# Performance work log

Hardware: AMD Instinct MI355X
Metric: run time of the kernel (lower is better)

## Reference

```python
import jax, jax.numpy as jnp
import numpy as np

B, D, N, K = 4, 1024, 2048, 1024
INIT_STD = 0.05  # keras 'random_normal' initializer default stddev


def setup_inputs() -> dict:
    key = jax.random.key(0)
    kx, kq, kk, kv, ko = jax.random.split(key, 5)
    inputs = jax.random.normal(kx, (B, D, N), dtype=jnp.float32)
    W_Q = jax.random.normal(kq, (K, D), dtype=jnp.float32) * INIT_STD
    W_K = jax.random.normal(kk, (K, D), dtype=jnp.float32) * INIT_STD
    W_V = jax.random.normal(kv, (K, D), dtype=jnp.float32) * INIT_STD
    W_O = jax.random.normal(ko, (K, D), dtype=jnp.float32) * INIT_STD
    return {"inputs": inputs, "W_Q": W_Q, "W_K": W_K, "W_V": W_V, "W_O": W_O}


def reference(inputs, W_Q, W_K, W_V, W_O):
    # inputs: (b, d, n) -- feature-major layout, sequence on the last axis.
    b, d, n = inputs.shape
    # Q/K projections fused into a single bilinear form: (W_Q x_i) . (W_K x_j)
    # logits[b, i, j] = x[:, i]^T W_Q^T W_K x[:, j]
    q = jnp.einsum('kd,bdi->bki', W_Q, inputs)          # (b, k, n)
    kk = jnp.einsum('kd,bdj->bkj', W_K, inputs)         # (b, k, n)
    logits = jnp.einsum('bki,bkj->bij', q, kk)          # (b, n, n)
    # Causal mask D: -inf strictly above the diagonal (query i attends j <= i).
    causal = jnp.tril(jnp.ones((n, n), dtype=bool))
    logits = jnp.where(causal, logits, -jnp.inf)
    A = jax.nn.softmax(logits, axis=-1)                 # (b, n_q, n_k)
    # context[:, :, i] = sum_t x[:, :, t] * A[i, t]
    ctx = jnp.einsum('bet,bit->bei', inputs, A)         # (b, d, n)
    # Residual + fused V/O projection: x + W_O^T W_V x A
    out = inputs + jnp.einsum('kd,ke,bei->bdi', W_O, W_V, ctx)
    return out
```

## Files before the change

kernel.cpp:

```cpp
#include <hip/hip_runtime.h>
#include <hip/hip_bf16.h>
#include <math.h>

#define BB 4
#define DD 1024
#define NN 2048
#define KK 1024
#define NT128 16
#define NTRI 136
#define TRI_ELEMS 16384

typedef __attribute__((ext_vector_type(4))) float f32x4;
typedef __attribute__((ext_vector_type(8))) short bfrag;

typedef __attribute__((address_space(1))) const unsigned int gu32;
typedef __attribute__((address_space(3))) unsigned int lu32;

__device__ __forceinline__ void async16(const void* g, void* l) {
  __builtin_amdgcn_global_load_lds((gu32*)g, (lu32*)l, 16, 0, 0);
}

__device__ __forceinline__ ushort f2b(float f) {
  union { float f; unsigned u; } c; c.f = f;
  unsigned u = c.u + 0x7fffu + ((c.u >> 16) & 1u);
  return (ushort)(u >> 16);
}
__device__ __forceinline__ float b2f(ushort h) {
  union { unsigned u; float f; } c; c.u = ((unsigned)h) << 16;
  return c.f;
}

__global__ __launch_bounds__(256) void prep(
    const float* __restrict__ x,
    const float* __restrict__ WQ, const float* __restrict__ WK,
    const float* __restrict__ WV, const float* __restrict__ WO,
    ushort* __restrict__ xhi, ushort* __restrict__ xTh, ushort* __restrict__ xTl,
    ushort* __restrict__ qh, ushort* __restrict__ ql,
    ushort* __restrict__ kh, ushort* __restrict__ kl_,
    ushort* __restrict__ vh, ushort* __restrict__ oh) {
  const int z = blockIdx.z;
  const int tx = threadIdx.x, ty = threadIdx.y;
  __shared__ float tile[32][33];
  if (z < 4) {
    const int b = z;
    const int n0 = blockIdx.x * 32, d0 = blockIdx.y * 32;
    const float* xb = x + (long)b * DD * NN;
    ushort* xhb = xhi + (long)b * DD * NN;
#pragma unroll
    for (int r = 0; r < 4; ++r) {
      const int dl = ty + r * 8;
      const float v = xb[(long)(d0 + dl) * NN + n0 + tx];
      tile[dl][tx] = v;
      xhb[(long)(d0 + dl) * NN + n0 + tx] = f2b(v);
    }
    __syncthreads();
#pragma unroll
    for (int r = 0; r < 4; ++r) {
      const int nl = ty + r * 8;
      const float v = tile[tx][nl];
      const ushort h = f2b(v);
      const long o = (long)b * NN * DD + (long)(n0 + nl) * DD + d0 + tx;
      xTh[o] = h;
      xTl[o] = f2b(v - b2f(h));
    }
  } else {
    const int w = (z - 4) * 2 + (blockIdx.x >> 5);
    const float* W = (w == 0) ? WQ : (w == 1) ? WK : (w == 2) ? WV : WO;
    ushort* Th = (w == 0) ? qh : (w == 1) ? kh : (w == 2) ? vh : oh;
    ushort* Tl = (w == 0) ? ql : (w == 1) ? kl_ : nullptr;
    const int k0 = (blockIdx.x & 31) * 32, d0 = blockIdx.y * 32;
#pragma unroll
    for (int r = 0; r < 4; ++r) {
      const int kl = ty + r * 8;
      tile[kl][tx] = W[(long)(k0 + kl) * DD + d0 + tx];
    }
    __syncthreads();
#pragma unroll
    for (int r = 0; r < 4; ++r) {
      const int dl = ty + r * 8;
      const float v = tile[tx][dl];
      const ushort h = f2b(v);
      const long o = (long)(d0 + dl) * KK + k0 + tx;
      Th[o] = h;
      if (Tl) Tl[o] = f2b(v - b2f(h));
    }
  }
}

__global__ __launch_bounds__(256) void gemm_w(
    const ushort* __restrict__ qh, const ushort* __restrict__ ql,
    const ushort* __restrict__ kh, const ushort* __restrict__ kl_,
    const ushort* __restrict__ vh, const ushort* __restrict__ oh,
    ushort* __restrict__ mqk_h, ushort* __restrict__ mqk_l,
    ushort* __restrict__ mov_h) {
  extern __shared__ ushort smem[];
  ushort* sAh = smem;
  ushort* sAl = smem + 2048;
  ushort* sBh = smem + 4096;
  ushort* sBl = smem + 6144;

  const int id = blockIdx.x;
  const int half = id >> 8;
  const int t = id & 255;
  const int m0 = (t >> 4) * 64, n0 = (t & 15) * 64;
  const ushort* A_h = half ? oh : qh;
  const ushort* B_h = half ? vh : kh;

  const int tid = threadIdx.x;
  const int lane = tid & 63, wave = tid >> 6;
  const int wm = (wave & 1) * 32, wn = (wave >> 1) * 32;
  const int r16 = lane & 15, quad = lane >> 4;
  const int kc = ((lane & 3) ^ ((lane >> 3) & 3)) * 8;
  const int srow = lane >> 2;

  f32x4 acc[2][2];
#pragma unroll
  for (int i = 0; i < 2; ++i)
#pragma unroll
    for (int j = 0; j < 2; ++j) acc[i][j] = (f32x4){0.f, 0.f, 0.f, 0.f};

  for (int k0 = 0; k0 < KK; k0 += 32) {
    __syncthreads();
    {
      const int row = wave * 16 + srow;
      const long aoff = (long)(m0 + row) * KK + k0 + kc;
      const long boff = (long)(n0 + row) * KK + k0 + kc;
      async16(A_h + aoff, sAh + wave * 512);
      async16(B_h + boff, sBh + wave * 512);
      if (half == 0) {
        async16(ql + aoff, sAl + wave * 512);
        async16(kl_ + boff, sBl + wave * 512);
      }
    }
    __syncthreads();

    const int sw = (r16 >> 1) & 3;
    bfrag ah[2], bh[2], al[2], bl[2];
#pragma unroll
    for (int t2 = 0; t2 < 2; ++t2) {
      ah[t2] = *(const bfrag*)&sAh[(wm + t2 * 16 + r16) * 32 + (quad ^ sw) * 8];
      bh[t2] = *(const bfrag*)&sBh[(wn + t2 * 16 + r16) * 32 + (quad ^ sw) * 8];
      if (half == 0) {
        al[t2] = *(const bfrag*)&sAl[(wm + t2 * 16 + r16) * 32 + (quad ^ sw) * 8];
        bl[t2] = *(const bfrag*)&sBl[(wn + t2 * 16 + r16) * 32 + (quad ^ sw) * 8];
      }
    }
#pragma unroll
    for (int mt = 0; mt < 2; ++mt)
#pragma unroll
      for (int nt = 0; nt < 2; ++nt) {
        acc[mt][nt] = __builtin_amdgcn_mfma_f32_16x16x32_bf16(ah[mt], bh[nt], acc[mt][nt], 0, 0, 0);
        if (half == 0) {
          acc[mt][nt] = __builtin_amdgcn_mfma_f32_16x16x32_bf16(ah[mt], bl[nt], acc[mt][nt], 0, 0, 0);
          acc[mt][nt] = __builtin_amdgcn_mfma_f32_16x16x32_bf16(al[mt], bh[nt], acc[mt][nt], 0, 0, 0);
        }
      }
  }

#pragma unroll
  for (int mt = 0; mt < 2; ++mt)
#pragma unroll
    for (int nt = 0; nt < 2; ++nt)
#pragma unroll
      for (int reg = 0; reg < 4; ++reg) {
        const int ml = wm + mt * 16 + quad * 4 + reg;
        const int nl = wn + nt * 16 + r16;
        const float v = acc[mt][nt][reg];
        const long o = (long)(m0 + ml) * DD + n0 + nl;
        if (half == 0) {
          const ushort h = f2b(v);
          mqk_h[o] = h;
          mqk_l[o] = f2b(v - b2f(h));
        } else {
          mov_h[o] = f2b(v);
        }
      }
}

template <int SPLIT, int TRIA, int STORE, int SWIZ>
__global__ __launch_bounds__(256) void gemm_mfma(
    const ushort* __restrict__ Ah, const ushort* __restrict__ Al,
    const ushort* __restrict__ Bh, const ushort* __restrict__ Bl,
    void* __restrict__ C0, void* __restrict__ C1, const float* __restrict__ Res,
    int K, int lda, int ldb, int ldc,
    long bA, long bB, long bC, long bR) {
  extern __shared__ ushort smem[];

  int b, m0, n0, tiC = 0;
  if (SWIZ == 2) {
    const int g = (blockIdx.x & 7) * 68 + (blockIdx.x >> 3);
    b = g / NTRI;
    int t = g - b * NTRI;
    int ti = 0;
    while ((ti + 1) * (ti + 2) / 2 <= t) ++ti;
    const int tj = t - ti * (ti + 1) / 2;
    m0 = ti * 128; n0 = tj * 128; tiC = t;
  } else if (SWIZ == 1) {
    const int g = (blockIdx.x & 7) * 64 + (blockIdx.x >> 3);
    const int P = g >> 3;
    b = P >> 4;
    m0 = (P & 15) * 128;
    n0 = (g & 7) * 128;
  } else if (SWIZ == 3) {
    const int xcd = blockIdx.x & 7;
    const int idx = blockIdx.x >> 3;
    const int q = idx >> 3;
    b = q >> 1;
    const int mt_ = (q & 1) ? (15 - xcd) : xcd;
    m0 = mt_ * 128;
    n0 = (idx & 7) * 128;
  } else {
    const int g = (blockIdx.x & 7) * 64 + (blockIdx.x >> 3);
    const int P = g >> 3;
    b = P >> 4;
    n0 = (P & 15) * 128;
    m0 = (g & 7) * 128;
  }
  const int kmax = TRIA ? (m0 + 128) : K;
  int triA0 = 0;
  if (TRIA) { const int ti = m0 >> 7; triA0 = ti * (ti + 1) / 2; }

  const ushort* A_h = Ah + (long)b * bA;
  const ushort* B_h = Bh + (long)b * bB;
  const ushort* A_l = SPLIT ? Al + (long)b * bA : nullptr;
  const ushort* B_l = SPLIT ? Bl + (long)b * bB : nullptr;

  const int tid = threadIdx.x;
  const int lane = tid & 63, wave = tid >> 6;
  const int wm = (wave & 1) * 64, wn = (wave >> 1) * 64;
  const int r16 = lane & 15, quad = lane >> 4;
  const int rk = r16 & 7;

  const int lrow = lane >> 3;
  const int lc = (lane & 7) ^ lrow;
  const int lckS = (lc & 3) * 8;
  const bool lo_src = lc >= 4;
  const int kcP = lc * 8;

  f32x4 acc[4][4];
#pragma unroll
  for (int i = 0; i < 4; ++i)
#pragma unroll
    for (int j = 0; j < 4; ++j) acc[i][j] = (f32x4){0.f, 0.f, 0.f, 0.f};

  auto STAGE = [&](int db, int t) {
    ushort* dst = smem + db * 16384;
    if (SPLIT) {
      const int k0 = t << 5;
#pragma unroll
      for (int s = 0; s < 4; ++s) {
        const int seg = wave * 4 + s;
        const int row = seg * 8 + lrow;
        const ushort* baseA = lo_src ? A_l : A_h;
        const ushort* baseB = lo_src ? B_l : B_h;
        async16(baseA + (long)(m0 + row) * lda + k0 + lckS, dst + seg * 512);
        async16(baseB + (long)(n0 + row) * ldb + k0 + lckS, dst + 8192 + seg * 512);
      }
    } else {
      const int k0 = t << 6;
#pragma unroll
      for (int s = 0; s < 4; ++s) {
        const int seg = wave * 4 + s;
        const int row = seg * 8 + lrow;
        long aoff;
        if (TRIA)
          aoff = (long)(triA0 + (k0 >> 7)) * TRI_ELEMS + (long)row * 128 + (k0 & 127) + kcP;
        else
          aoff = (long)(m0 + row) * lda + k0 + kcP;
        async16(A_h + aoff, dst + seg * 512);
        async16(B_h + (long)(n0 + row) * ldb + k0 + kcP, dst + 8192 + seg * 512);
      }
    }
  };

  const int T = kmax >> (SPLIT ? 5 : 6);
  STAGE(0, 0);
  asm volatile("s_waitcnt vmcnt(0)" ::: "memory");
  __builtin_amdgcn_s_barrier();
  __builtin_amdgcn_sched_barrier(0);

  for (int t = 0; t < T; ++t) {
    const int cur = t & 1;
    if (t + 1 < T) STAGE(cur ^ 1, t + 1);
    const ushort* sA = smem + cur * 16384;
    const ushort* sB = sA + 8192;

    if (SPLIT) {
      bfrag ah[4], al[4], bh[4], bl[4];
#pragma unroll
      for (int f = 0; f < 4; ++f) {
        const int arow = (wm + f * 16 + r16) * 64;
        const int brow = (wn + f * 16 + r16) * 64;
        ah[f] = *(const bfrag*)&sA[arow + (quad ^ rk) * 8];
        al[f] = *(const bfrag*)&sA[arow + ((quad + 4) ^ rk) * 8];
        bh[f] = *(const bfrag*)&sB[brow + (quad ^ rk) * 8];
        bl[f] = *(const bfrag*)&sB[brow + ((quad + 4) ^ rk) * 8];
      }
      __builtin_amdgcn_s_setprio(1);
#pragma unroll
      for (int mt = 0; mt < 4; ++mt)
#pragma unroll
        for (int nt = 0; nt < 4; ++nt) {
          acc[mt][nt] = __builtin_amdgcn_mfma_f32_16x16x32_bf16(ah[mt], bh[nt], acc[mt][nt], 0, 0, 0);
          acc[mt][nt] = __builtin_amdgcn_mfma_f32_16x16x32_bf16(ah[mt], bl[nt], acc[mt][nt], 0, 0, 0);
          acc[mt][nt] = __builtin_amdgcn_mfma_f32_16x16x32_bf16(al[mt], bh[nt], acc[mt][nt], 0, 0, 0);
        }
      __builtin_amdgcn_s_setprio(0);
    } else {
#pragma unroll
      for (int ksub = 0; ksub < 2; ++ksub) {
        const int ch = ((ksub * 4 + quad) ^ rk) * 8;
        bfrag a4[4], b4[4];
#pragma unroll
        for (int f = 0; f < 4; ++f) {
          a4[f] = *(const bfrag*)&sA[(wm + f * 16 + r16) * 64 + ch];
          b4[f] = *(const bfrag*)&sB[(wn + f * 16 + r16) * 64 + ch];
        }
        __builtin_amdgcn_s_setprio(1);
#pragma unroll
        for (int mt = 0; mt < 4; ++mt)
#pragma unroll
          for (int nt = 0; nt < 4; ++nt)
            acc[mt][nt] = __builtin_amdgcn_mfma_f32_16x16x32_bf16(a4[mt], b4[nt], acc[mt][nt], 0, 0, 0);
        __builtin_amdgcn_s_setprio(0);
      }
    }

    __builtin_amdgcn_sched_barrier(0);
    asm volatile("s_waitcnt vmcnt(0)" ::: "memory");
    __builtin_amdgcn_s_barrier();
    __builtin_amdgcn_sched_barrier(0);
  }

#pragma unroll
  for (int mt = 0; mt < 4; ++mt)
#pragma unroll
    for (int nt = 0; nt < 4; ++nt)
#pragma unroll
      for (int reg = 0; reg < 4; ++reg) {
        const int ml = wm + mt * 16 + quad * 4 + reg;
        const int nl = wn + nt * 16 + r16;
        const float v = acc[mt][nt][reg];
        if (STORE == 0) {
          ushort* Ch = (ushort*)C0 + (long)b * bC;
          ushort* Cl = (ushort*)C1 + (long)b * bC;
          const long o = (long)(m0 + ml) * ldc + n0 + nl;
          const ushort h = f2b(v);
          Ch[o] = h;
          Cl[o] = f2b(v - b2f(h));
        } else if (STORE == 1) {
          float* C = (float*)C0 + (long)b * bC + (long)tiC * TRI_ELEMS;
          C[ml * 128 + nl] = v;
        } else if (STORE == 2) {
          ushort* C = (ushort*)C0 + (long)b * bC;
          C[(long)(m0 + ml) * ldc + n0 + nl] = f2b(v);
        } else {
          float* C = (float*)C0 + (long)b * bC;
          const float* R = Res + (long)b * bR;
          const long o = (long)(m0 + ml) * ldc + n0 + nl;
          C[o] = R[o] + v;
        }
      }
}

__global__ __launch_bounds__(256) void softmax_tri(
    const float* __restrict__ L, ushort* __restrict__ Aout) {
  const int row = blockIdx.x;
  const int b = row >> 11, i = row & (NN - 1);
  const int ti = i >> 7, ml = i & 127;
  const long base = (long)b * ((long)NTRI * TRI_ELEMS);
  const int trib = ti * (ti + 1) / 2;
  const int len = i + 1;
  const int tot = (ti + 1) * 128;
  const int tid = threadIdx.x;
  __shared__ float red[256];
  float vv[8];
  float m = -INFINITY;
#pragma unroll
  for (int u = 0; u < 8; ++u) {
    const int j = tid + u * 256;
    if (j < len) {
      const float v = L[base + (long)(trib + (j >> 7)) * TRI_ELEMS + ml * 128 + (j & 127)];
      vv[u] = v;
      m = fmaxf(m, v);
    }
  }
  red[tid] = m; __syncthreads();
  for (int s = 128; s; s >>= 1) { if (tid < s) red[tid] = fmaxf(red[tid], red[tid + s]); __syncthreads(); }
  m = red[0]; __syncthreads();
  float sum = 0.f;
#pragma unroll
  for (int u = 0; u < 8; ++u) {
    const int j = tid + u * 256;
    if (j < len) { const float e = __expf(vv[u] - m); vv[u] = e; sum += e; }
  }
  red[tid] = sum; __syncthreads();
  for (int s = 128; s; s >>= 1) { if (tid < s) red[tid] += red[tid + s]; __syncthreads(); }
  const float inv = 1.f / red[0];
#pragma unroll
  for (int u = 0; u < 8; ++u) {
    const int j = tid + u * 256;
    if (j < tot) {
      const ushort o = (j < len) ? f2b(vv[u] * inv) : (ushort)0;
      Aout[base + (long)(trib + (j >> 7)) * TRI_ELEMS + ml * 128 + (j & 127)] = o;
    }
  }
}

extern "C" void kernel_launch(void* const* d_in, const int* in_sizes, int n_in,
                              void* d_out, int out_size, void* d_ws, size_t ws_size,
                              hipStream_t stream) {
  const float* x = (const float*)d_in[0];
  const float* WQ = (const float*)d_in[1];
  const float* WK = (const float*)d_in[2];
  const float* WV = (const float*)d_in[3];
  const float* WO = (const float*)d_in[4];
  float* out = (float*)d_out;

  const long XE = (long)BB * DD * NN;
  const long WE = (long)DD * KK;
  ushort* x_hi = (ushort*)d_ws;
  ushort* xTh = x_hi + XE;
  ushort* xTl = xTh + XE;
  ushort* wqT_h = xTl + XE;
  ushort* wqT_l = wqT_h + WE;
  ushort* wkT_h = wqT_l + WE;
  ushort* wkT_l = wkT_h + WE;
  ushort* wvT_h = wkT_l + WE;
  ushort* woT_h = wvT_h + WE;
  ushort* mqk_h = woT_h + WE;
  ushort* mqk_l = mqk_h + WE;
  ushort* mov_h = mqk_l + WE;
  ushort* tTh = mov_h + WE;
  ushort* tTl = tTh + XE;
  float* logits = (float*)(tTl + XE);
  ushort* A_tri = tTh;
  ushort* ctxT = (ushort*)logits;
  const long TRIB = (long)NTRI * TRI_ELEMS;
  const long XB = XE / BB;

  prep<<<dim3(64, 32, 6), dim3(32, 8), 0, stream>>>(
      x, WQ, WK, WV, WO, x_hi, xTh, xTl,
      wqT_h, wqT_l, wkT_h, wkT_l, wvT_h, woT_h);

  gemm_w<<<dim3(512), 256, 16384, stream>>>(
      wqT_h, wqT_l, wkT_h, wkT_l, wvT_h, woT_h, mqk_h, mqk_l, mov_h);

  gemm_mfma<1, 0, 0, 1><<<dim3(512), 256, 65536, stream>>>(
      xTh, xTl, mqk_h, mqk_l, tTh, tTl, nullptr,
      DD, DD, DD, DD, XB, 0, XB, 0);

  gemm_mfma<1, 0, 1, 2><<<dim3(BB * NTRI), 256, 65536, stream>>>(
      xTh, xTl, tTh, tTl, logits, nullptr, nullptr,
      DD, DD, DD, 0, XB, XB, TRIB, 0);

  softmax_tri<<<dim3(BB * NN), 256, 0, stream>>>(logits, A_tri);

  gemm_mfma<0, 1, 2, 3><<<dim3(512), 256, 65536, stream>>>(
      A_tri, nullptr, x_hi, nullptr, ctxT, nullptr, nullptr,
      NN, 0, NN, DD, TRIB, XB, XB, 0);

  gemm_mfma<0, 0, 3, 4><<<dim3(512), 256, 65536, stream>>>(
      mov_h, nullptr, ctxT, nullptr, out, nullptr, x,
      DD, DD, DD, NN, 0, XB, XB, XB);
}
```

Before: 327.6 us.

## Use 256x128 tiles with 8 waves and triple-buffered pipeline for split-bf16 GEMMs

The two split-precision GEMMs (x·Mqk and the triangular logits) move to a new kernel with 512 threads, 256x128 output tiles and a three-stage LDS ring that prefetches two K-steps ahead. The three hi/lo product passes are run as sequential K-phases (48 steps) instead of interleaved within each step. The logits kernel covers 256-row bands, so it computes some upper-triangle tiles that are discarded at store time. The aim is more data reuse per tile and better latency hiding, at the price of more LDS per block, lower occupancy and some wasted triangular work.

```diff
diff --git a/kernel.cpp b/kernel.cpp
--- a/kernel.cpp
+++ b/kernel.cpp
@@ -177,31 +177,145 @@
       }
 }
 
-template <int SPLIT, int TRIA, int STORE, int SWIZ>
-__global__ __launch_bounds__(256) void gemm_mfma(
+template <int MODE>
+__global__ __launch_bounds__(512) void gemm8(
     const ushort* __restrict__ Ah, const ushort* __restrict__ Al,
     const ushort* __restrict__ Bh, const ushort* __restrict__ Bl,
-    void* __restrict__ C0, void* __restrict__ C1, const float* __restrict__ Res,
+    void* __restrict__ C0, void* __restrict__ C1,
+    int lda, int ldb, int ldc, long bA, long bB, long bC) {
+  __shared__ ushort smem[73728];
+
+  int b, m0, n0, jt = 0;
+  if (MODE == 0) {
+    const int g = (blockIdx.x & 7) * 32 + (blockIdx.x >> 3);
+    const int mt = g >> 3;
+    b = mt >> 3;
+    m0 = (mt & 7) * 256;
+    n0 = (g & 7) * 128;
+  } else {
+    const int g = (blockIdx.x & 7) * 36 + (blockIdx.x >> 3);
+    b = g / 72;
+    const int r = g - b * 72;
+    int I = 0;
+    while ((I + 1) * (I + 2) <= r) ++I;
+    jt = r - I * (I + 1);
+    m0 = I * 256;
+    n0 = jt * 128;
+  }
+
+  const ushort* A_hb = Ah + (long)b * bA;
+  const ushort* A_lb = Al + (long)b * bA;
+  const ushort* B_hb = Bh + (long)b * bB;
+  const ushort* B_lb = Bl + (long)b * bB;
+
+  const int tid = threadIdx.x;
+  const int lane = tid & 63, wave = tid >> 6;
+  const int wm = (wave & 3) * 64, wn = (wave >> 2) * 64;
+  const int r16 = lane & 15, quad = lane >> 4;
+  const int rk = r16 & 7;
+
+  const int lrow = lane >> 3;
+  const int lc = (lane & 7) ^ lrow;
+  const int kc = lc * 8;
+
+  f32x4 acc[4][4];
+#pragma unroll
+  for (int i = 0; i < 4; ++i)
+#pragma unroll
+    for (int j = 0; j < 4; ++j) acc[i][j] = (f32x4){0.f, 0.f, 0.f, 0.f};
+
+  auto STAGE = [&](int db, int t, int h) {
+    const int third = t >> 4;
+    const int k0 = (t & 15) << 6;
+    const ushort* A = (third == 1) ? A_lb : A_hb;
+    const ushort* B = (third == 2) ? B_lb : B_hb;
+    ushort* dst = smem + db * 24576;
+#pragma unroll
+    for (int s = 0; s < 2; ++s) {
+      const int seg = wave * 4 + h * 2 + s;
+      const int row = seg * 8 + lrow;
+      async16(A + (long)(m0 + row) * lda + k0 + kc, dst + seg * 512);
+    }
+    {
+      const int seg = wave * 2 + h;
+      const int row = seg * 8 + lrow;
+      async16(B + (long)(n0 + row) * ldb + k0 + kc, dst + 16384 + seg * 512);
+    }
+  };
+
+  const int T = 48;
+  STAGE(0, 0, 0); STAGE(0, 0, 1);
+  STAGE(1, 1, 0); STAGE(1, 1, 1);
+
+  for (int t = 0; t < T; ++t) {
+    const int cur = t % 3;
+    if (t + 1 < T) asm volatile("s_waitcnt vmcnt(6)" ::: "memory");
+    else           asm volatile("s_waitcnt vmcnt(0)" ::: "memory");
+    __builtin_amdgcn_s_barrier();
+    __builtin_amdgcn_sched_barrier(0);
+
+    const ushort* sA = smem + cur * 24576;
+    const ushort* sB = sA + 16384;
+#pragma unroll
+    for (int ks = 0; ks < 2; ++ks) {
+      const int ch = ((ks * 4 + quad) ^ rk) * 8;
+      bfrag a4[4], b4[4];
+#pragma unroll
+      for (int f = 0; f < 4; ++f) {
+        a4[f] = *(const bfrag*)&sA[(wm + f * 16 + r16) * 64 + ch];
+        b4[f] = *(const bfrag*)&sB[(wn + f * 16 + r16) * 64 + ch];
+      }
+      if (t + 2 < T) STAGE((t + 2) % 3, t + 2, ks);
+      asm volatile("s_waitcnt lgkmcnt(0)" ::: "memory");
+      __builtin_amdgcn_sched_barrier(0);
+      __builtin_amdgcn_s_setprio(1);
+#pragma unroll
+      for (int mt = 0; mt < 4; ++mt)
+#pragma unroll
+        for (int nt = 0; nt < 4; ++nt)
+          acc[mt][nt] = __builtin_amdgcn_mfma_f32_16x16x32_bf16(a4[mt], b4[nt], acc[mt][nt], 0, 0, 0);
+      __builtin_amdgcn_s_setprio(0);
+      if (ks == 0) __builtin_amdgcn_s_barrier();
+    }
+  }
+
+#pragma unroll
+  for (int mt = 0; mt < 4; ++mt)
+#pragma unroll
+    for (int nt = 0; nt < 4; ++nt)
+#pragma unroll
+      for (int reg = 0; reg < 4; ++reg) {
+        const int ml = wm + mt * 16 + quad * 4 + reg;
+        const int nl = wn + nt * 16 + r16;
+        const float v = acc[mt][nt][reg];
+        if (MODE == 0) {
+          ushort* Ch = (ushort*)C0 + (long)b * bC;
+          ushort* Cl = (ushort*)C1 + (long)b * bC;
+          const long o = (long)(m0 + ml) * ldc + n0 + nl;
+          const ushort h = f2b(v);
+          Ch[o] = h;
+          Cl[o] = f2b(v - b2f(h));
+        } else {
+          const int gi = m0 + ml;
+          const int ti = gi >> 7;
+          if (jt <= ti) {
+            float* C = (float*)C0 + (long)b * bC;
+            C[(long)(ti * (ti + 1) / 2 + jt) * TRI_ELEMS + (gi & 127) * 128 + nl] = v;
+          }
+        }
+      }
+}
+
+template <int TRIA, int STORE, int SWIZ>
+__global__ __launch_bounds__(256) void gemm_mfma(
+    const ushort* __restrict__ Ah, const ushort* __restrict__ Bh,
+    void* __restrict__ C0, const float* __restrict__ Res,
     int K, int lda, int ldb, int ldc,
     long bA, long bB, long bC, long bR) {
   extern __shared__ ushort smem[];
 
-  int b, m0, n0, tiC = 0;
-  if (SWIZ == 2) {
-    const int g = (blockIdx.x & 7) * 68 + (blockIdx.x >> 3);
-    b = g / NTRI;
-    int t = g - b * NTRI;
-    int ti = 0;
-    while ((ti + 1) * (ti + 2) / 2 <= t) ++ti;
-    const int tj = t - ti * (ti + 1) / 2;
-    m0 = ti * 128; n0 = tj * 128; tiC = t;
-  } else if (SWIZ == 1) {
-    const int g = (blockIdx.x & 7) * 64 + (blockIdx.x >> 3);
-    const int P = g >> 3;
-    b = P >> 4;
-    m0 = (P & 15) * 128;
-    n0 = (g & 7) * 128;
-  } else if (SWIZ == 3) {
+  int b, m0, n0;
+  if (SWIZ == 3) {
     const int xcd = blockIdx.x & 7;
     const int idx = blockIdx.x >> 3;
     const int q = idx >> 3;
@@ -222,8 +336,6 @@
 
   const ushort* A_h = Ah + (long)b * bA;
   const ushort* B_h = Bh + (long)b * bB;
-  const ushort* A_l = SPLIT ? Al + (long)b * bA : nullptr;
-  const ushort* B_l = SPLIT ? Bl + (long)b * bB : nullptr;
 
   const int tid = threadIdx.x;
   const int lane = tid & 63, wave = tid >> 6;
@@ -233,8 +345,6 @@
 
   const int lrow = lane >> 3;
   const int lc = (lane & 7) ^ lrow;
-  const int lckS = (lc & 3) * 8;
-  const bool lo_src = lc >= 4;
   const int kcP = lc * 8;
 
   f32x4 acc[4][4];
@@ -245,35 +355,22 @@
 
   auto STAGE = [&](int db, int t) {
     ushort* dst = smem + db * 16384;
-    if (SPLIT) {
-      const int k0 = t << 5;
-#pragma unroll
-      for (int s = 0; s < 4; ++s) {
-        const int seg = wave * 4 + s;
-        const int row = seg * 8 + lrow;
-        const ushort* baseA = lo_src ? A_l : A_h;
-        const ushort* baseB = lo_src ? B_l : B_h;
-        async16(baseA + (long)(m0 + row) * lda + k0 + lckS, dst + seg * 512);
-        async16(baseB + (long)(n0 + row) * ldb + k0 + lckS, dst + 8192 + seg * 512);
-      }
-    } else {
-      const int k0 = t << 6;
-#pragma unroll
-      for (int s = 0; s < 4; ++s) {
-        const int seg = wave * 4 + s;
-        const int row = seg * 8 + lrow;
-        long aoff;
-        if (TRIA)
-          aoff = (long)(triA0 + (k0 >> 7)) * TRI_ELEMS + (long)row * 128 + (k0 & 127) + kcP;
-        else
-          aoff = (long)(m0 + row) * lda + k0 + kcP;
-        async16(A_h + aoff, dst + seg * 512);
-        async16(B_h + (long)(n0 + row) * ldb + k0 + kcP, dst + 8192 + seg * 512);
-      }
+    const int k0 = t << 6;
+#pragma unroll
+    for (int s = 0; s < 4; ++s) {
+      const int seg = wave * 4 + s;
+      const int row = seg * 8 + lrow;
+      long aoff;
+      if (TRIA)
+        aoff = (long)(triA0 + (k0 >> 7)) * TRI_ELEMS + (long)row * 128 + (k0 & 127) + kcP;
+      else
+        aoff = (long)(m0 + row) * lda + k0 + kcP;
+      async16(A_h + aoff, dst + seg * 512);
+      async16(B_h + (long)(n0 + row) * ldb + k0 + kcP, dst + 8192 + seg * 512);
     }
   };
 
-  const int T = kmax >> (SPLIT ? 5 : 6);
+  const int T = kmax >> 6;
   STAGE(0, 0);
   asm volatile("s_waitcnt vmcnt(0)" ::: "memory");
   __builtin_amdgcn_s_barrier();
@@ -285,45 +382,22 @@
     const ushort* sA = smem + cur * 16384;
     const ushort* sB = sA + 8192;
 
-    if (SPLIT) {
-      bfrag ah[4], al[4], bh[4], bl[4];
+#pragma unroll
+    for (int ksub = 0; ksub < 2; ++ksub) {
+      const int ch = ((ksub * 4 + quad) ^ rk) * 8;
+      bfrag a4[4], b4[4];
 #pragma unroll
       for (int f = 0; f < 4; ++f) {
-        const int arow = (wm + f * 16 + r16) * 64;
-        const int brow = (wn + f * 16 + r16) * 64;
-        ah[f] = *(const bfrag*)&sA[arow + (quad ^ rk) * 8];
-        al[f] = *(const bfrag*)&sA[arow + ((quad + 4) ^ rk) * 8];
-        bh[f] = *(const bfrag*)&sB[brow + (quad ^ rk) * 8];
-        bl[f] = *(const bfrag*)&sB[brow + ((quad + 4) ^ rk) * 8];
+        a4[f] = *(const bfrag*)&sA[(wm + f * 16 + r16) * 64 + ch];
+        b4[f] = *(const bfrag*)&sB[(wn + f * 16 + r16) * 64 + ch];
       }
       __builtin_amdgcn_s_setprio(1);
 #pragma unroll
       for (int mt = 0; mt < 4; ++mt)
 #pragma unroll
-        for (int nt = 0; nt < 4; ++nt) {
-          acc[mt][nt] = __builtin_amdgcn_mfma_f32_16x16x32_bf16(ah[mt], bh[nt], acc[mt][nt], 0, 0, 0);
-          acc[mt][nt] = __builtin_amdgcn_mfma_f32_16x16x32_bf16(ah[mt], bl[nt], acc[mt][nt], 0, 0, 0);
-          acc[mt][nt] = __builtin_amdgcn_mfma_f32_16x16x32_bf16(al[mt], bh[nt], acc[mt][nt], 0, 0, 0);
-        }
+        for (int nt = 0; nt < 4; ++nt)
+          acc[mt][nt] = __builtin_amdgcn_mfma_f32_16x16x32_bf16(a4[mt], b4[nt], acc[mt][nt], 0, 0, 0);
       __builtin_amdgcn_s_setprio(0);
-    } else {
-#pragma unroll
-      for (int ksub = 0; ksub < 2; ++ksub) {
-        const int ch = ((ksub * 4 + quad) ^ rk) * 8;
-        bfrag a4[4], b4[4];
-#pragma unroll
-        for (int f = 0; f < 4; ++f) {
-          a4[f] = *(const bfrag*)&sA[(wm + f * 16 + r16) * 64 + ch];
-          b4[f] = *(const bfrag*)&sB[(wn + f * 16 + r16) * 64 + ch];
-        }
-        __builtin_amdgcn_s_setprio(1);
-#pragma unroll
-        for (int mt = 0; mt < 4; ++mt)
-#pragma unroll
-          for (int nt = 0; nt < 4; ++nt)
-            acc[mt][nt] = __builtin_amdgcn_mfma_f32_16x16x32_bf16(a4[mt], b4[nt], acc[mt][nt], 0, 0, 0);
-        __builtin_amdgcn_s_setprio(0);
-      }
     }
 
     __builtin_amdgcn_sched_barrier(0);
@@ -341,17 +415,7 @@
         const int ml = wm + mt * 16 + quad * 4 + reg;
         const int nl = wn + nt * 16 + r16;
         const float v = acc[mt][nt][reg];
-        if (STORE == 0) {
-          ushort* Ch = (ushort*)C0 + (long)b * bC;
-          ushort* Cl = (ushort*)C1 + (long)b * bC;
-          const long o = (long)(m0 + ml) * ldc + n0 + nl;
-          const ushort h = f2b(v);
-          Ch[o] = h;
-          Cl[o] = f2b(v - b2f(h));
-        } else if (STORE == 1) {
-          float* C = (float*)C0 + (long)b * bC + (long)tiC * TRI_ELEMS;
-          C[ml * 128 + nl] = v;
-        } else if (STORE == 2) {
+        if (STORE == 2) {
           ushort* C = (ushort*)C0 + (long)b * bC;
           C[(long)(m0 + ml) * ldc + n0 + nl] = f2b(v);
         } else {
@@ -446,21 +510,21 @@
   gemm_w<<<dim3(512), 256, 16384, stream>>>(
       wqT_h, wqT_l, wkT_h, wkT_l, wvT_h, woT_h, mqk_h, mqk_l, mov_h);
 
-  gemm_mfma<1, 0, 0, 1><<<dim3(512), 256, 65536, stream>>>(
-      xTh, xTl, mqk_h, mqk_l, tTh, tTl, nullptr,
-      DD, DD, DD, DD, XB, 0, XB, 0);
-
-  gemm_mfma<1, 0, 1, 2><<<dim3(BB * NTRI), 256, 65536, stream>>>(
-      xTh, xTl, tTh, tTl, logits, nullptr, nullptr,
-      DD, DD, DD, 0, XB, XB, TRIB, 0);
+  gemm8<0><<<dim3(256), dim3(512), 0, stream>>>(
+      xTh, xTl, mqk_h, mqk_l, tTh, tTl,
+      DD, DD, DD, XB, 0, XB);
+
+  gemm8<1><<<dim3(288), dim3(512), 0, stream>>>(
+      xTh, xTl, tTh, tTl, logits, nullptr,
+      DD, DD, 0, XB, XB, TRIB);
 
   softmax_tri<<<dim3(BB * NN), 256, 0, stream>>>(logits, A_tri);
 
-  gemm_mfma<0, 1, 2, 3><<<dim3(512), 256, 65536, stream>>>(
-      A_tri, nullptr, x_hi, nullptr, ctxT, nullptr, nullptr,
+  gemm_mfma<1, 2, 3><<<dim3(512), 256, 65536, stream>>>(
+      A_tri, x_hi, ctxT, nullptr,
       NN, 0, NN, DD, TRIB, XB, XB, 0);
 
-  gemm_mfma<0, 0, 3, 4><<<dim3(512), 256, 65536, stream>>>(
-      mov_h, nullptr, ctxT, nullptr, out, nullptr, x,
+  gemm_mfma<0, 3, 4><<<dim3(512), 256, 65536, stream>>>(
+      mov_h, ctxT, out, x,
       DD, DD, DD, NN, 0, XB, XB, XB);
 }
```

Measured after the change: 339.4 us. 3.6% more time.
